# Kernel optimization log

Measured on AMD Instinct MI355X. Metric: run time of the kernel, lower is better.

The kernel has to match this reference:

```python
import jax, jax.numpy as jnp
import numpy as np
from jax import lax

N_PER_GRAPH = 64   # nodes per graph (dest = last node)
N_GRAPHS = 8192
DEG = 8            # out-edges per non-dest node
N_FEATS = 4
NEG = -1e9         # finite stand-in for -inf (avoids inf/nan in grads)


def _build_dag_edges():
    # node i in a graph gets DEG edges to random j in (i, N-1]; acyclic -> Bellman-Ford converges
    rng = np.random.default_rng(0)
    i = np.repeat(np.arange(N_PER_GRAPH - 1), DEG)            # [ (N-1)*DEG ]
    span = N_PER_GRAPH - 1 - i
    tgt_local = i + 1 + (rng.random((N_GRAPHS, i.size)) * span).astype(np.int64)
    off = (np.arange(N_GRAPHS, dtype=np.int64) * N_PER_GRAPH)[:, None]
    src = np.broadcast_to(i[None, :], (N_GRAPHS, i.size)) + off
    tgt = tgt_local + off
    return np.stack([src.reshape(-1), tgt.reshape(-1)])       # [2, E]


def setup_inputs() -> dict:
    key = jax.random.key(0)
    k1, k2 = jax.random.split(key, 2)
    n_nodes = N_GRAPHS * N_PER_GRAPH
    edge_index = jnp.asarray(_build_dag_edges())               # [2, E] int64
    n_edges = edge_index.shape[1]
    feats = jax.random.normal(k1, (n_edges, N_FEATS), jnp.float32) * 0.5
    dest_mask = (jnp.arange(n_nodes) % N_PER_GRAPH) == (N_PER_GRAPH - 1)
    W = jax.random.normal(k2, (1, N_FEATS), jnp.float32) * 0.5  # Linear(n_feats,1).weight
    b = jnp.zeros((1,), jnp.float32)                            # Linear bias (link_constant)
    return {"feats": feats, "dest_mask": dest_mask, "edge_index": edge_index,
            "W": W, "b": b, "n_steps": N_PER_GRAPH - 1}


def reference(feats, dest_mask, edge_index, W, b, n_steps):
    # util = coeffs(feats): per-edge scalar utility, shape [E,1]
    n_nodes = dest_mask.shape[0]
    util = feats @ W.T + b                                     # [E,1]
    src, tgt = edge_index[0], edge_index[1]                    # flow='target_to_source': aggregate into src
    value0 = jnp.where(dest_mask[:, None], 0.0, NEG)           # [n_nodes,1]; dest pinned at 0

    def step(value, _):
        msg = value[tgt] + util                                # gather value_j + util per edge
        agg = jax.ops.segment_max(msg, src, num_segments=n_nodes)  # scatter-max into source nodes
        agg = jnp.maximum(agg, NEG)                            # empty segments: -inf -> NEG
        value = jnp.where(dest_mask[:, None], 0.0, agg)        # dest stays 0
        return value, None

    value, _ = lax.scan(step, value0, None, length=n_steps)    # n_steps = max nodes/graph - 1
    return value, util
```

## Files before the change

### kernel.cpp

```cpp
#include <hip/hip_runtime.h>

#define NEGV (-1.0e9f)
constexpr int NODES = 64;
constexpr int EPG   = 504;
constexpr int STEPS = 63;

__global__ __launch_bounds__(256)
void rl_sweep_kernel(const float* __restrict__ feats,
                     const int*   __restrict__ edge_tgt,
                     const float* __restrict__ Wp,
                     const float* __restrict__ bp,
                     float*       __restrict__ out_value,
                     float*       __restrict__ out_util,
                     int n_graphs)
{
    const int wid  = (blockIdx.x * blockDim.x + threadIdx.x) >> 6;
    const int lane = threadIdx.x & 63;
    if (wid >= n_graphs) return;

    const float w0 = Wp[0], w1 = Wp[1], w2 = Wp[2], w3 = Wp[3];
    const float bb = bp[0];

    const long eb = (long)wid * EPG;

    float4 f[8];
    int    t[8];
#pragma unroll
    for (int j = 7; j >= 0; --j) {
        const int e = j * 64 + lane;
        if (e < EPG) {
            f[j] = *reinterpret_cast<const float4*>(feats + (eb + e) * 4);
            t[j] = (edge_tgt[eb + e] & (NODES - 1)) << 2;
        } else {
            f[j] = make_float4(0.f, 0.f, 0.f, 0.f);
            t[j] = 0;
        }
    }

    float u[8];
#pragma unroll
    for (int j = 7; j >= 0; --j)
        u[j] = f[j].x * w0 + f[j].y * w1 + f[j].z * w2 + f[j].w * w3 + bb;

    float value = (lane == NODES - 1) ? 0.0f : NEGV;

#pragma unroll
    for (int i = STEPS - 1; i >= 0; --i) {
        const int r = i >> 3;
        const int m = i & 7;

        const float vt  = __int_as_float(
            __builtin_amdgcn_ds_bpermute(t[r], __float_as_int(value)));
        float msg = vt + u[r];

        msg = fmaxf(msg, __int_as_float(__builtin_amdgcn_update_dpp(
                          0, __float_as_int(msg), 0xB1, 0xF, 0xF, true)));
        msg = fmaxf(msg, __int_as_float(__builtin_amdgcn_update_dpp(
                          0, __float_as_int(msg), 0x4E, 0xF, 0xF, true)));
        msg = fmaxf(msg, __int_as_float(__builtin_amdgcn_update_dpp(
                          0, __float_as_int(msg), 0x141, 0xF, 0xF, true)));

        const float red = __int_as_float(
            __builtin_amdgcn_readlane(__float_as_int(msg), 8 * m));
        value = (lane == i) ? red : value;
    }

    __builtin_nontemporal_store(value, out_value + (long)wid * NODES + lane);
#pragma unroll
    for (int j = 0; j < 8; ++j) {
        const int e = j * 64 + lane;
        if (e < EPG)
            __builtin_nontemporal_store(u[j], out_util + eb + e);
    }
}

extern "C" void kernel_launch(void* const* d_in, const int* in_sizes, int n_in,
                              void* d_out, int out_size, void* d_ws, size_t ws_size,
                              hipStream_t stream)
{
    const float* feats      = (const float*)d_in[0];
    const int*   edge_index = (const int*)d_in[2];
    const float* W          = (const float*)d_in[3];
    const float* b          = (const float*)d_in[4];

    const int E        = in_sizes[0] / 4;
    const int n_nodes  = in_sizes[1];
    const int n_graphs = n_nodes / NODES;

    float* out_value = (float*)d_out;
    float* out_util  = out_value + n_nodes;
    const int* edge_tgt = edge_index + E;

    const int total = n_graphs * 64;
    const int block = 256;
    const int grid  = (total + block - 1) / block;
    rl_sweep_kernel<<<grid, block, 0, stream>>>(feats, edge_tgt, W, b,
                                                out_value, out_util, n_graphs);
}
```

Before: 21.98 us.

## Overlap per-row edge loads with sweep steps using staged waitcnt

Issues all edge target and feature loads up front with no predication, clamping out-of-range indices to the last edge. Each group of eight sweep steps waits only for its own row's loads through an explicit vmcnt wait, so the early steps can run while the later rows' loads are still in flight. Utility and target-index math move inside each stage. Scheduling barriers pin the load order, which the hand-written vmcnt counts depend on, and this limits what the compiler can reorder.

```diff
diff --git a/kernel.cpp b/kernel.cpp
--- a/kernel.cpp
+++ b/kernel.cpp
@@ -12,7 +12,7 @@
                      const float* __restrict__ bp,
                      float*       __restrict__ out_value,
                      float*       __restrict__ out_util,
-                     int n_graphs)
+                     int n_graphs, int E)
 {
     const int wid  = (blockIdx.x * blockDim.x + threadIdx.x) >> 6;
     const int lane = threadIdx.x & 63;
@@ -20,52 +20,54 @@
 
     const float w0 = Wp[0], w1 = Wp[1], w2 = Wp[2], w3 = Wp[3];
     const float bb = bp[0];
+    const unsigned eb = (unsigned)wid * (unsigned)EPG;
 
-    const long eb = (long)wid * EPG;
-
+    int    traw[8];
     float4 f[8];
-    int    t[8];
 #pragma unroll
     for (int j = 7; j >= 0; --j) {
-        const int e = j * 64 + lane;
-        if (e < EPG) {
-            f[j] = *reinterpret_cast<const float4*>(feats + (eb + e) * 4);
-            t[j] = (edge_tgt[eb + e] & (NODES - 1)) << 2;
-        } else {
-            f[j] = make_float4(0.f, 0.f, 0.f, 0.f);
-            t[j] = 0;
-        }
+        unsigned idx = eb + (unsigned)(j * 64 + lane);
+        if (idx >= (unsigned)E) idx = (unsigned)(E - 1);
+        traw[j] = edge_tgt[idx];
+        f[j]    = *reinterpret_cast<const float4*>(feats + (size_t)idx * 4u);
+        __builtin_amdgcn_sched_barrier(0);
     }
 
+    float value = (lane == NODES - 1) ? 0.0f : NEGV;
     float u[8];
-#pragma unroll
-    for (int j = 7; j >= 0; --j)
-        u[j] = f[j].x * w0 + f[j].y * w1 + f[j].z * w2 + f[j].w * w3 + bb;
-
-    float value = (lane == NODES - 1) ? 0.0f : NEGV;
 
 #pragma unroll
-    for (int i = STEPS - 1; i >= 0; --i) {
-        const int r = i >> 3;
-        const int m = i & 7;
+    for (int r = 7; r >= 0; --r) {
+        asm volatile("s_waitcnt vmcnt(%0)" :: "i"(2 * r) : "memory");
+        __builtin_amdgcn_sched_barrier(0);
 
-        const float vt  = __int_as_float(
-            __builtin_amdgcn_ds_bpermute(t[r], __float_as_int(value)));
-        float msg = vt + u[r];
+        u[r] = f[r].x * w0 + f[r].y * w1 + f[r].z * w2 + f[r].w * w3 + bb;
+        const int tr = (traw[r] & (NODES - 1)) << 2;
 
-        msg = fmaxf(msg, __int_as_float(__builtin_amdgcn_update_dpp(
-                          0, __float_as_int(msg), 0xB1, 0xF, 0xF, true)));
-        msg = fmaxf(msg, __int_as_float(__builtin_amdgcn_update_dpp(
-                          0, __float_as_int(msg), 0x4E, 0xF, 0xF, true)));
-        msg = fmaxf(msg, __int_as_float(__builtin_amdgcn_update_dpp(
-                          0, __float_as_int(msg), 0x141, 0xF, 0xF, true)));
+        const int hi = (r == 7) ? (STEPS - 1) : (r * 8 + 7);
+#pragma unroll
+        for (int i = hi; i >= r * 8; --i) {
+            const int m = i & 7;
 
-        const float red = __int_as_float(
-            __builtin_amdgcn_readlane(__float_as_int(msg), 8 * m));
-        value = (lane == i) ? red : value;
+            const float vt = __int_as_float(
+                __builtin_amdgcn_ds_bpermute(tr, __float_as_int(value)));
+            float msg = vt + u[r];
+
+            msg = fmaxf(msg, __int_as_float(__builtin_amdgcn_update_dpp(
+                              0, __float_as_int(msg), 0xB1, 0xF, 0xF, true)));
+            msg = fmaxf(msg, __int_as_float(__builtin_amdgcn_update_dpp(
+                              0, __float_as_int(msg), 0x4E, 0xF, 0xF, true)));
+            msg = fmaxf(msg, __int_as_float(__builtin_amdgcn_update_dpp(
+                              0, __float_as_int(msg), 0x141, 0xF, 0xF, true)));
+
+            const float red = __int_as_float(
+                __builtin_amdgcn_readlane(__float_as_int(msg), 8 * m));
+            value = (lane == i) ? red : value;
+        }
+        __builtin_amdgcn_sched_barrier(0);
     }
 
-    __builtin_nontemporal_store(value, out_value + (long)wid * NODES + lane);
+    __builtin_nontemporal_store(value, out_value + (size_t)wid * NODES + lane);
 #pragma unroll
     for (int j = 0; j < 8; ++j) {
         const int e = j * 64 + lane;
@@ -95,5 +97,5 @@
     const int block = 256;
     const int grid  = (total + block - 1) / block;
     rl_sweep_kernel<<<grid, block, 0, stream>>>(feats, edge_tgt, W, b,
-                                                out_value, out_util, n_graphs);
+                                                out_value, out_util, n_graphs, E);
 }
```

After: 24.51 us. +11.5%, slower.
